# Kernel optimization log

Measured on AMD Instinct MI355X. Metric: run time of the kernel, lower is better.

The kernel has to match this reference:

```python
import jax, jax.numpy as jnp
import numpy as np

H, W = 128, 128
TANFOVX = 0.5
TANFOVY = 0.5
SCALE_MOD = 1.0
NEAR = 0.2
N = 2048


def setup_inputs() -> dict:
    key = jax.random.key(0)
    ks = jax.random.split(key, 6)
    # Gaussians in front of an identity camera looking down +z
    xy = jax.random.uniform(ks[0], (N, 2), minval=-1.5, maxval=1.5)
    z = jax.random.uniform(ks[1], (N, 1), minval=2.5, maxval=6.5)
    means3D = jnp.concatenate([xy, z], axis=1).astype(jnp.float32)
    opacities = jax.random.uniform(ks[2], (N, 1), minval=0.05, maxval=0.95)
    colors_precomp = jax.random.uniform(ks[3], (N, 3))
    scales = jax.random.uniform(ks[4], (N, 3), minval=0.01, maxval=0.06)
    rotations = jax.random.normal(ks[5], (N, 4))
    viewmatrix = jnp.eye(4, dtype=jnp.float32)  # world == camera frame
    bg = jnp.zeros((3,), dtype=jnp.float32)
    return dict(means3D=means3D, opacities=opacities,
                colors_precomp=colors_precomp, scales=scales,
                rotations=rotations, viewmatrix=viewmatrix, bg=bg)


def _quat_to_rot(q):
    # normalized quaternion (w, x, y, z) -> rotation matrix, as in the CUDA kernel
    q = q / jnp.linalg.norm(q, axis=-1, keepdims=True)
    w, x, y, z = q[:, 0], q[:, 1], q[:, 2], q[:, 3]
    return jnp.stack([
        jnp.stack([1 - 2 * (y * y + z * z), 2 * (x * y - w * z), 2 * (x * z + w * y)], -1),
        jnp.stack([2 * (x * y + w * z), 1 - 2 * (x * x + z * z), 2 * (y * z - w * x)], -1),
        jnp.stack([2 * (x * z - w * y), 2 * (y * z + w * x), 1 - 2 * (x * x + y * y)], -1),
    ], -2)  # [N,3,3]


def _forward(means3D, opacities, colors_precomp, scales, rotations, viewmatrix, bg):
    fx = W / (2.0 * TANFOVX)
    fy = H / (2.0 * TANFOVY)
    Rv = viewmatrix[:3, :3]
    tv = viewmatrix[:3, 3]
    pv = means3D @ Rv.T + tv            # view-space positions [N,3]
    x, y, z = pv[:, 0], pv[:, 1], pv[:, 2]
    zc = jnp.maximum(z, 1e-4)
    # frustum clamping of the EWA Jacobian, as in forward.cu
    tx = jnp.clip(x / zc, -1.3 * TANFOVX, 1.3 * TANFOVX) * zc
    ty = jnp.clip(y / zc, -1.3 * TANFOVY, 1.3 * TANFOVY) * zc
    zeros = jnp.zeros_like(zc)
    J = jnp.stack([
        jnp.stack([fx / zc, zeros, -fx * tx / (zc * zc)], -1),
        jnp.stack([zeros, fy / zc, -fy * ty / (zc * zc)], -1),
    ], -2)                               # [N,2,3]
    # 3D covariance Sigma = R S S^T R^T
    Rg = _quat_to_rot(rotations)
    M = Rg * (scales * SCALE_MOD)[:, None, :]
    Sigma = M @ jnp.swapaxes(M, -1, -2)  # [N,3,3]
    T2 = jnp.einsum('nij,jk->nik', J, Rv)
    cov2d = jnp.einsum('nij,njk,nlk->nil', T2, Sigma, T2)
    a = cov2d[:, 0, 0] + 0.3             # low-pass filter, as in CUDA
    b = cov2d[:, 0, 1]
    c = cov2d[:, 1, 1] + 0.3
    det = a * c - b * b
    valid = (det > 0) & (z > NEAR)
    inv_det = jnp.where(det != 0, 1.0 / det, 0.0)
    conA, conB, conC = c * inv_det, -b * inv_det, a * inv_det
    mid = 0.5 * (a + c)
    lam = mid + jnp.sqrt(jnp.maximum(mid * mid - det, 0.1))
    radii = jnp.where(valid, jnp.ceil(3.0 * jnp.sqrt(lam)), 0.0)
    # projected pixel-space means
    mx = fx * (x / zc) + 0.5 * (W - 1)
    my = fy * (y / zc) + 0.5 * (H - 1)

    # global front-to-back depth sort (CUDA sorts per tile; one tile here)
    order = jnp.argsort(z)
    mx_s, my_s = mx[order], my[order]
    A_s, B_s, C_s = conA[order], conB[order], conC[order]
    op_s = opacities[order, 0]
    z_s = z[order]
    col_s = colors_precomp[order]
    valid_s = valid[order]

    px = jnp.arange(W, dtype=means3D.dtype)
    py = jnp.arange(H, dtype=means3D.dtype)
    Dx = mx_s[None, :] - px[:, None]     # [W,N]
    Dy = my_s[None, :] - py[:, None]     # [H,N]
    # power = -0.5 (A dx^2 + C dy^2) - B dx dy, built [H,W,N]
    power = (-0.5 * A_s * Dx * Dx)[None, :, :] \
            + (-0.5 * C_s * Dy * Dy)[:, None, :] \
            - (B_s * Dx)[None, :, :] * Dy[:, None, :]
    alpha = jnp.minimum(0.99, op_s * jnp.exp(jnp.minimum(power, 0.0)))
    alpha = jnp.where((power <= 0.0) & valid_s & (alpha >= 1.0 / 255.0), alpha, 0.0)
    alpha = alpha.reshape(H * W, N)      # [HW,N], front-to-back order
    logt = jnp.log1p(-alpha)
    csum = jnp.cumsum(logt, axis=-1)
    T_excl = jnp.exp(csum - logt)        # exclusive transmittance prod_{j<i}(1-a_j)
    wgt = alpha * T_excl                 # compositing weights
    T_final = jnp.exp(csum[:, -1])
    color = jnp.einsum('pn,nc->cp', wgt, col_s).reshape(3, H, W) \
            + T_final.reshape(1, H, W) * bg[:, None, None]
    depth = (wgt * z_s[None, :]).sum(-1).reshape(H, W)
    alpha_img = (1.0 - T_final).reshape(H, W)
    return color, radii, depth, alpha_img


def reference(means3D, opacities, colors_precomp, scales, rotations, viewmatrix, bg):
    return _forward(means3D, opacities, colors_precomp, scales, rotations, viewmatrix, bg)
```

## Files before the change

### kernel.cpp

```cpp
#include <hip/hip_runtime.h>

#define NG    2048
#define IMG_W 128
#define IMG_H 128
#define NPIX  (IMG_W * IMG_H)
#define KCAP  768

__global__ __launch_bounds__(256) void fused_raster_kernel(
    const float* __restrict__ means,
    const float* __restrict__ opac,
    const float* __restrict__ cols,
    const float* __restrict__ scales,
    const float* __restrict__ rots,
    const float* __restrict__ vm4,
    const float* __restrict__ bg,
    float* __restrict__ out)
{
    __shared__ unsigned short cand[NG];
    __shared__ float recs[KCAP][10];
    __shared__ float pz[KCAP];
    __shared__ unsigned short pid[KCAP];
    __shared__ unsigned short perm[KCAP];
    __shared__ float comb[4 * 64 * 5];
    __shared__ int cntM, cntK;

    int tid  = threadIdx.x;
    int tile = blockIdx.x;
    int x0 = (tile & 15) * 8;
    int y0 = (tile >> 4) * 8;
    float x0f = (float)x0,       y0f = (float)y0;
    float x1f = (float)(x0 + 7), y1f = (float)(y0 + 7);

    if (tid == 0) { cntM = 0; cntK = 0; }
    __syncthreads();

    float fR00 = vm4[0], fR01 = vm4[1], fR02 = vm4[2],  ft0 = vm4[3];
    float fR10 = vm4[4], fR11 = vm4[5], fR12 = vm4[6],  ft1 = vm4[7];
    float fR20 = vm4[8], fR21 = vm4[9], fR22 = vm4[10], ft2 = vm4[11];

    if (tid >= 64) {
        float r0s = fabsf(fR00) + fabsf(fR01) + fabsf(fR02);
        float r1s = fabsf(fR10) + fabsf(fR11) + fabsf(fR12);
        float r2s = fabsf(fR20) + fabsf(fR21) + fabsf(fR22);
        float c0s = fabsf(fR00) + fabsf(fR10) + fabsf(fR20);
        float c1s = fabsf(fR01) + fabsf(fR11) + fabsf(fR21);
        float c2s = fabsf(fR02) + fabsf(fR12) + fabsf(fR22);
        float r2norm = fmaxf(r0s, fmaxf(r1s, r2s)) * fmaxf(c0s, fmaxf(c1s, c2s));

        for (int g = tid - 64; g < NG; g += 192) {
            float m0 = means[3*g+0], m1 = means[3*g+1], m2 = means[3*g+2];
            float x = fR00*m0 + fR01*m1 + fR02*m2 + ft0;
            float y = fR10*m0 + fR11*m1 + fR12*m2 + ft1;
            float z = fR20*m0 + fR21*m1 + fR22*m2 + ft2;
            float zc = fmaxf(z, 1e-4f);
            float invz = 1.0f / zc;
            float xi = x * invz, yi = y * invz;
            float mx = 128.f * xi + 63.5f;
            float my = 128.f * yi + 63.5f;
            float txc = fminf(0.65f, fmaxf(-0.65f, xi));
            float tyc = fminf(0.65f, fmaxf(-0.65f, yi));
            float jf = 128.f * invz;
            float frJ = jf * jf * (2.f + txc*txc + tyc*tyc);
            float s0 = scales[3*g+0], s1 = scales[3*g+1], s2 = scales[3*g+2];
            float smax2 = fmaxf(s0*s0, fmaxf(s1*s1, s2*s2));
            float lnterm = __logf(255.f * opac[g]);
            bool maybe = false;
            if (lnterm > 0.f) {
                float lam_pf = frJ * r2norm * smax2 * 1.02f + 0.95f;
                float r2 = 2.f * lnterm * lam_pf * 1.02f + 1.0f;
                float ddx = fmaxf(0.f, fmaxf(x0f - mx, mx - x1f));
                float ddy = fmaxf(0.f, fmaxf(y0f - my, my - y1f));
                maybe = (ddx*ddx + ddy*ddy) <= r2;
            }
            if (maybe) {
                int s = atomicAdd(&cntM, 1);
                cand[s] = (unsigned short)g;
            }
        }
    } else if (tid < 8) {
        int i = tile * 8 + tid;
        double R00 = vm4[0], R01 = vm4[1], R02 = vm4[2];
        double R10 = vm4[4], R11 = vm4[5], R12 = vm4[6];
        double R20 = vm4[8], R21 = vm4[9], R22 = vm4[10];
        double t2d = vm4[11];
        double m0 = means[3*i+0], m1 = means[3*i+1], m2 = means[3*i+2];
        double x = R00*m0 + R01*m1 + R02*m2 + (double)vm4[3];
        double y = R10*m0 + R11*m1 + R12*m2 + (double)vm4[7];
        double z = R20*m0 + R21*m1 + R22*m2 + t2d;
        double zc   = fmax(z, 1e-4);
        double invz = 1.0 / zc;
        double tx = fmin(0.65, fmax(-0.65, x * invz)) * zc;
        double ty = fmin(0.65, fmax(-0.65, y * invz)) * zc;
        double J00 = 128.0 * invz, J02 = -128.0 * tx * invz * invz;
        double J11 = 128.0 * invz, J12 = -128.0 * ty * invz * invz;
        double qw = rots[4*i+0], qx = rots[4*i+1], qy = rots[4*i+2], qz = rots[4*i+3];
        double qn = 1.0 / sqrt(qw*qw + qx*qx + qy*qy + qz*qz);
        qw *= qn; qx *= qn; qy *= qn; qz *= qn;
        double Rg00 = 1.0-2.0*(qy*qy+qz*qz), Rg01 = 2.0*(qx*qy-qw*qz), Rg02 = 2.0*(qx*qz+qw*qy);
        double Rg10 = 2.0*(qx*qy+qw*qz), Rg11 = 1.0-2.0*(qx*qx+qz*qz), Rg12 = 2.0*(qy*qz-qw*qx);
        double Rg20 = 2.0*(qx*qz-qw*qy), Rg21 = 2.0*(qy*qz+qw*qx), Rg22 = 1.0-2.0*(qx*qx+qy*qy);
        double s0 = scales[3*i+0], s1 = scales[3*i+1], s2 = scales[3*i+2];
        double M00 = Rg00*s0, M01 = Rg01*s1, M02 = Rg02*s2;
        double M10 = Rg10*s0, M11 = Rg11*s1, M12 = Rg12*s2;
        double M20 = Rg20*s0, M21 = Rg21*s1, M22 = Rg22*s2;
        double S00 = M00*M00+M01*M01+M02*M02;
        double S01 = M00*M10+M01*M11+M02*M12;
        double S02 = M00*M20+M01*M21+M02*M22;
        double S11 = M10*M10+M11*M11+M12*M12;
        double S12 = M10*M20+M11*M21+M12*M22;
        double S22 = M20*M20+M21*M21+M22*M22;
        double Ta0 = J00*R00+J02*R20, Ta1 = J00*R01+J02*R21, Ta2 = J00*R02+J02*R22;
        double Tb0 = J11*R10+J12*R20, Tb1 = J11*R11+J12*R21, Tb2 = J11*R12+J12*R22;
        double Ua0 = Ta0*S00+Ta1*S01+Ta2*S02;
        double Ua1 = Ta0*S01+Ta1*S11+Ta2*S12;
        double Ua2 = Ta0*S02+Ta1*S12+Ta2*S22;
        double Ub0 = Tb0*S00+Tb1*S01+Tb2*S02;
        double Ub1 = Tb0*S01+Tb1*S11+Tb2*S12;
        double Ub2 = Tb0*S02+Tb1*S12+Tb2*S22;
        double a = Ua0*Ta0+Ua1*Ta1+Ua2*Ta2 + 0.3;
        double b = Ua0*Tb0+Ua1*Tb1+Ua2*Tb2;
        double c = Ub0*Tb0+Ub1*Tb1+Ub2*Tb2 + 0.3;
        double det = a*c - b*b;
        bool valid = (det > 0.0) && (z > 0.2);
        double mid = 0.5 * (a + c);
        double lam = mid + sqrt(fmax(mid*mid - det, 0.1));
        out[3*NPIX + i] = valid ? (float)ceil(3.0 * sqrt(lam)) : 0.0f;
    }
    __syncthreads();
    int M = cntM;

    for (int k = tid; k < M; k += 256) {
        int gi = cand[k];
        float m0 = means[3*gi+0], m1 = means[3*gi+1], m2 = means[3*gi+2];
        double zd = (double)vm4[8]*m0 + (double)vm4[9]*m1 + (double)vm4[10]*m2 + (double)vm4[11];
        float z = (float)zd;
        float x = fR00*m0 + fR01*m1 + fR02*m2 + ft0;
        float y = fR10*m0 + fR11*m1 + fR12*m2 + ft1;
        float zc = fmaxf(z, 1e-4f);
        float invz = 1.0f / zc;
        float tx = fminf(0.65f, fmaxf(-0.65f, x * invz)) * zc;
        float ty = fminf(0.65f, fmaxf(-0.65f, y * invz)) * zc;
        float J00 = 128.f * invz, J02 = -128.f * tx * invz * invz;
        float J11 = 128.f * invz, J12 = -128.f * ty * invz * invz;
        float qw = rots[4*gi+0], qx = rots[4*gi+1], qy = rots[4*gi+2], qz = rots[4*gi+3];
        float qn = 1.0f / sqrtf(qw*qw + qx*qx + qy*qy + qz*qz);
        qw *= qn; qx *= qn; qy *= qn; qz *= qn;
        float Rg00 = 1.f-2.f*(qy*qy+qz*qz), Rg01 = 2.f*(qx*qy-qw*qz), Rg02 = 2.f*(qx*qz+qw*qy);
        float Rg10 = 2.f*(qx*qy+qw*qz), Rg11 = 1.f-2.f*(qx*qx+qz*qz), Rg12 = 2.f*(qy*qz-qw*qx);
        float Rg20 = 2.f*(qx*qz-qw*qy), Rg21 = 2.f*(qy*qz+qw*qx), Rg22 = 1.f-2.f*(qx*qx+qy*qy);
        float s0 = scales[3*gi+0], s1 = scales[3*gi+1], s2 = scales[3*gi+2];
        float M00 = Rg00*s0, M01 = Rg01*s1, M02 = Rg02*s2;
        float M10 = Rg10*s0, M11 = Rg11*s1, M12 = Rg12*s2;
        float M20 = Rg20*s0, M21 = Rg21*s1, M22 = Rg22*s2;
        float S00 = M00*M00+M01*M01+M02*M02;
        float S01 = M00*M10+M01*M11+M02*M12;
        float S02 = M00*M20+M01*M21+M02*M22;
        float S11 = M10*M10+M11*M11+M12*M12;
        float S12 = M10*M20+M11*M21+M12*M22;
        float S22 = M20*M20+M21*M21+M22*M22;
        float Ta0 = J00*fR00+J02*fR20, Ta1 = J00*fR01+J02*fR21, Ta2 = J00*fR02+J02*fR22;
        float Tb0 = J11*fR10+J12*fR20, Tb1 = J11*fR11+J12*fR21, Tb2 = J11*fR12+J12*fR22;
        float Ua0 = Ta0*S00+Ta1*S01+Ta2*S02;
        float Ua1 = Ta0*S01+Ta1*S11+Ta2*S12;
        float Ua2 = Ta0*S02+Ta1*S12+Ta2*S22;
        float Ub0 = Tb0*S00+Tb1*S01+Tb2*S02;
        float Ub1 = Tb0*S01+Tb1*S11+Tb2*S12;
        float Ub2 = Tb0*S02+Tb1*S12+Tb2*S22;
        float a = Ua0*Ta0+Ua1*Ta1+Ua2*Ta2 + 0.3f;
        float b = Ua0*Tb0+Ua1*Tb1+Ua2*Tb2;
        float c = Ub0*Tb0+Ub1*Tb1+Ub2*Tb2 + 0.3f;
        float det = a*c - b*b;
        bool valid = (det > 0.0f) && (z > 0.2f);
        float inv_det = (det != 0.0f) ? (1.0f / det) : 0.0f;
        float mid = 0.5f * (a + c);
        float lam = mid + sqrtf(fmaxf(mid*mid - det, 0.1f));
        float op = valid ? opac[gi] : 0.0f;
        float r2c = -1.0f;
        if (op > 0.0f) {
            float lnterm = __logf(255.f * op);
            if (lnterm > 0.0f) r2c = 2.f * lnterm * lam * 1.001f + 1e-2f;
        }
        float fmx = 128.f * (x * invz) + 63.5f;
        float fmy = 128.f * (y * invz) + 63.5f;
        float ddx = fmaxf(0.f, fmaxf(x0f - fmx, fmx - x1f));
        float ddy = fmaxf(0.f, fmaxf(y0f - fmy, fmy - y1f));
        if (ddx*ddx + ddy*ddy <= r2c) {
            int s = atomicAdd(&cntK, 1);
            if (s < KCAP) {
                recs[s][0] = fmx;
                recs[s][1] = fmy;
                recs[s][2] =  c * inv_det;
                recs[s][3] = -b * inv_det;
                recs[s][4] =  a * inv_det;
                recs[s][5] = op;
                recs[s][6] = z;
                recs[s][7] = cols[3*gi+0];
                recs[s][8] = cols[3*gi+1];
                recs[s][9] = cols[3*gi+2];
                pz[s]  = z;
                pid[s] = (unsigned short)gi;
            }
        }
    }
    __syncthreads();
    int K = min(cntK, KCAP);

    for (int r = tid; r < K; r += 256) {
        float zr = pz[r];
        int ir = pid[r];
        int rank = 0;
        for (int s2 = 0; s2 < K; ++s2)
            rank += (pz[s2] < zr) || (pz[s2] == zr && pid[s2] < ir);
        perm[rank] = (unsigned short)r;
    }
    __syncthreads();

    int lane = tid & 63;
    int w    = tid >> 6;
    int px = x0 + (lane & 7);
    int py = y0 + (lane >> 3);
    float fpx = (float)px, fpy = (float)py;
    int p = py * IMG_W + px;

    int q  = (K + 3) >> 2;
    int rs = w * q;
    int re = min(rs + q, K);

    float cr = 0.f, cg = 0.f, cb = 0.f, dep = 0.f, T = 1.f;
    for (int r = rs; r < re; ++r) {
        const float* rr = recs[perm[r]];
        float dx = rr[0] - fpx;
        float dy = rr[1] - fpy;
        float power = -0.5f * (rr[2]*dx*dx + rr[4]*dy*dy) - rr[3]*dx*dy;
        float al = fminf(0.99f, rr[5] * __expf(power));
        bool take = (power <= 0.0f) && (al >= (1.0f / 255.0f));
        float wgt = take ? al * T : 0.0f;
        dep += wgt * rr[6];
        cr  += wgt * rr[7];
        cg  += wgt * rr[8];
        cb  += wgt * rr[9];
        if (take) T *= (1.0f - al);
    }

    int cb_base = (w * 64 + lane) * 5;
    comb[cb_base + 0] = cr;
    comb[cb_base + 1] = cg;
    comb[cb_base + 2] = cb;
    comb[cb_base + 3] = dep;
    comb[cb_base + 4] = T;
    __syncthreads();

    if (w == 0) {
        float CR = 0.f, CG = 0.f, CB = 0.f, DEP = 0.f, TT = 1.f;
        #pragma unroll
        for (int ww = 0; ww < 4; ++ww) {
            int b2 = (ww * 64 + lane) * 5;
            CR  += TT * comb[b2 + 0];
            CG  += TT * comb[b2 + 1];
            CB  += TT * comb[b2 + 2];
            DEP += TT * comb[b2 + 3];
            TT  *= comb[b2 + 4];
        }
        out[0*NPIX + p] = CR + TT * bg[0];
        out[1*NPIX + p] = CG + TT * bg[1];
        out[2*NPIX + p] = CB + TT * bg[2];
        out[3*NPIX + NG + p]        = DEP;
        out[3*NPIX + NG + NPIX + p] = 1.f - TT;
    }
}

extern "C" void kernel_launch(void* const* d_in, const int* in_sizes, int n_in,
                              void* d_out, int out_size, void* d_ws, size_t ws_size,
                              hipStream_t stream)
{
    const float* means = (const float*)d_in[0];
    const float* opac  = (const float*)d_in[1];
    const float* cols  = (const float*)d_in[2];
    const float* scl   = (const float*)d_in[3];
    const float* rot   = (const float*)d_in[4];
    const float* vm    = (const float*)d_in[5];
    const float* bg    = (const float*)d_in[6];
    float* out = (float*)d_out;

    fused_raster_kernel<<<256, 256, 0, stream>>>(
        means, opac, cols, scl, rot, vm, bg, out);
}
```

Before: 23.80 us.

## Drop conservative prefilter pass and scatter sorted records into padded float4 array

Removes the separate candidate-culling pass that ran on 192 threads with an atomic-appended candidate list. All 256 threads now run the full per-Gaussian projection directly over all 2048 Gaussians. The depth sort now copies each record into a second padded 12-float array at its rank, so the compositing loop reads three contiguous float4 values without an index indirection. The cost is full projection work for every Gaussian instead of a prefiltered subset, plus a larger shared-memory footprint that may reduce occupancy.

Measured after the change: 24.32 us. +2.2%, slower.

```diff
diff --git a/kernel.cpp b/kernel.cpp
--- a/kernel.cpp
+++ b/kernel.cpp
@@ -16,13 +16,12 @@
     const float* __restrict__ bg,
     float* __restrict__ out)
 {
-    __shared__ unsigned short cand[NG];
-    __shared__ float recs[KCAP][10];
+    __shared__ __align__(16) float recs[KCAP][12];
+    __shared__ __align__(16) float srec[KCAP][12];
     __shared__ float pz[KCAP];
     __shared__ unsigned short pid[KCAP];
-    __shared__ unsigned short perm[KCAP];
     __shared__ float comb[4 * 64 * 5];
-    __shared__ int cntM, cntK;
+    __shared__ int cntK;
 
     int tid  = threadIdx.x;
     int tile = blockIdx.x;
@@ -31,62 +30,22 @@
     float x0f = (float)x0,       y0f = (float)y0;
     float x1f = (float)(x0 + 7), y1f = (float)(y0 + 7);
 
-    if (tid == 0) { cntM = 0; cntK = 0; }
+    if (tid == 0) cntK = 0;
     __syncthreads();
 
     float fR00 = vm4[0], fR01 = vm4[1], fR02 = vm4[2],  ft0 = vm4[3];
     float fR10 = vm4[4], fR11 = vm4[5], fR12 = vm4[6],  ft1 = vm4[7];
     float fR20 = vm4[8], fR21 = vm4[9], fR22 = vm4[10], ft2 = vm4[11];
 
-    if (tid >= 64) {
-        float r0s = fabsf(fR00) + fabsf(fR01) + fabsf(fR02);
-        float r1s = fabsf(fR10) + fabsf(fR11) + fabsf(fR12);
-        float r2s = fabsf(fR20) + fabsf(fR21) + fabsf(fR22);
-        float c0s = fabsf(fR00) + fabsf(fR10) + fabsf(fR20);
-        float c1s = fabsf(fR01) + fabsf(fR11) + fabsf(fR21);
-        float c2s = fabsf(fR02) + fabsf(fR12) + fabsf(fR22);
-        float r2norm = fmaxf(r0s, fmaxf(r1s, r2s)) * fmaxf(c0s, fmaxf(c1s, c2s));
-
-        for (int g = tid - 64; g < NG; g += 192) {
-            float m0 = means[3*g+0], m1 = means[3*g+1], m2 = means[3*g+2];
-            float x = fR00*m0 + fR01*m1 + fR02*m2 + ft0;
-            float y = fR10*m0 + fR11*m1 + fR12*m2 + ft1;
-            float z = fR20*m0 + fR21*m1 + fR22*m2 + ft2;
-            float zc = fmaxf(z, 1e-4f);
-            float invz = 1.0f / zc;
-            float xi = x * invz, yi = y * invz;
-            float mx = 128.f * xi + 63.5f;
-            float my = 128.f * yi + 63.5f;
-            float txc = fminf(0.65f, fmaxf(-0.65f, xi));
-            float tyc = fminf(0.65f, fmaxf(-0.65f, yi));
-            float jf = 128.f * invz;
-            float frJ = jf * jf * (2.f + txc*txc + tyc*tyc);
-            float s0 = scales[3*g+0], s1 = scales[3*g+1], s2 = scales[3*g+2];
-            float smax2 = fmaxf(s0*s0, fmaxf(s1*s1, s2*s2));
-            float lnterm = __logf(255.f * opac[g]);
-            bool maybe = false;
-            if (lnterm > 0.f) {
-                float lam_pf = frJ * r2norm * smax2 * 1.02f + 0.95f;
-                float r2 = 2.f * lnterm * lam_pf * 1.02f + 1.0f;
-                float ddx = fmaxf(0.f, fmaxf(x0f - mx, mx - x1f));
-                float ddy = fmaxf(0.f, fmaxf(y0f - my, my - y1f));
-                maybe = (ddx*ddx + ddy*ddy) <= r2;
-            }
-            if (maybe) {
-                int s = atomicAdd(&cntM, 1);
-                cand[s] = (unsigned short)g;
-            }
-        }
-    } else if (tid < 8) {
+    if (tid < 8) {
         int i = tile * 8 + tid;
         double R00 = vm4[0], R01 = vm4[1], R02 = vm4[2];
         double R10 = vm4[4], R11 = vm4[5], R12 = vm4[6];
         double R20 = vm4[8], R21 = vm4[9], R22 = vm4[10];
-        double t2d = vm4[11];
         double m0 = means[3*i+0], m1 = means[3*i+1], m2 = means[3*i+2];
         double x = R00*m0 + R01*m1 + R02*m2 + (double)vm4[3];
         double y = R10*m0 + R11*m1 + R12*m2 + (double)vm4[7];
-        double z = R20*m0 + R21*m1 + R22*m2 + t2d;
+        double z = R20*m0 + R21*m1 + R22*m2 + (double)vm4[11];
         double zc   = fmax(z, 1e-4);
         double invz = 1.0 / zc;
         double tx = fmin(0.65, fmax(-0.65, x * invz)) * zc;
@@ -126,11 +85,10 @@
         double lam = mid + sqrt(fmax(mid*mid - det, 0.1));
         out[3*NPIX + i] = valid ? (float)ceil(3.0 * sqrt(lam)) : 0.0f;
     }
-    __syncthreads();
-    int M = cntM;
-
-    for (int k = tid; k < M; k += 256) {
-        int gi = cand[k];
+
+    #pragma unroll 2
+    for (int it = 0; it < NG / 256; ++it) {
+        int gi = it * 256 + tid;
         float m0 = means[3*gi+0], m1 = means[3*gi+1], m2 = means[3*gi+2];
         double zd = (double)vm4[8]*m0 + (double)vm4[9]*m1 + (double)vm4[10]*m2 + (double)vm4[11];
         float z = (float)zd;
@@ -211,7 +169,12 @@
         int rank = 0;
         for (int s2 = 0; s2 < K; ++s2)
             rank += (pz[s2] < zr) || (pz[s2] == zr && pid[s2] < ir);
-        perm[rank] = (unsigned short)r;
+        float4 v0 = ((const float4*)recs[r])[0];
+        float4 v1 = ((const float4*)recs[r])[1];
+        float4 v2 = ((const float4*)recs[r])[2];
+        ((float4*)srec[rank])[0] = v0;
+        ((float4*)srec[rank])[1] = v1;
+        ((float4*)srec[rank])[2] = v2;
     }
     __syncthreads();
 
@@ -228,17 +191,19 @@
 
     float cr = 0.f, cg = 0.f, cb = 0.f, dep = 0.f, T = 1.f;
     for (int r = rs; r < re; ++r) {
-        const float* rr = recs[perm[r]];
-        float dx = rr[0] - fpx;
-        float dy = rr[1] - fpy;
-        float power = -0.5f * (rr[2]*dx*dx + rr[4]*dy*dy) - rr[3]*dx*dy;
-        float al = fminf(0.99f, rr[5] * __expf(power));
+        float4 v0 = ((const float4*)srec[r])[0];
+        float4 v1 = ((const float4*)srec[r])[1];
+        float4 v2 = ((const float4*)srec[r])[2];
+        float dx = v0.x - fpx;
+        float dy = v0.y - fpy;
+        float power = -0.5f * (v0.z*dx*dx + v1.x*dy*dy) - v0.w*dx*dy;
+        float al = fminf(0.99f, v1.y * __expf(power));
         bool take = (power <= 0.0f) && (al >= (1.0f / 255.0f));
         float wgt = take ? al * T : 0.0f;
-        dep += wgt * rr[6];
-        cr  += wgt * rr[7];
-        cg  += wgt * rr[8];
-        cb  += wgt * rr[9];
+        dep += wgt * v1.z;
+        cr  += wgt * v1.w;
+        cg  += wgt * v2.x;
+        cb  += wgt * v2.y;
         if (take) T *= (1.0f - al);
     }
 
```
